# Kernel optimization log

Hardware: AMD Instinct MI355X
Metric: run time of the kernel (lower is better)

Reference implementation:

```python
import jax, jax.numpy as jnp
import numpy as np

N_NODES = 50000
N_EDGES = 600000
HIDDEN = 128
OUT = 64


def gcn_conv(x, edge_index, W, b, num_nodes):
    """PyG GCNConv: out = D^-1/2 (A+I) D^-1/2 (x W) + b, deg computed on A+I."""
    src, dst = edge_index[0], edge_index[1]
    loops = jnp.arange(num_nodes, dtype=src.dtype)
    src_f = jnp.concatenate([src, loops])  # [E+N]
    dst_f = jnp.concatenate([dst, loops])
    deg = jax.ops.segment_sum(jnp.ones_like(dst_f, dtype=x.dtype), dst_f,
                              num_segments=num_nodes)  # in-degree incl. self-loop
    dinv = jnp.where(deg > 0, jax.lax.rsqrt(deg), 0.0)
    norm = dinv[src_f] * dinv[dst_f]  # [E+N]
    xw = x @ W  # [N, out]
    msg = xw[src_f] * norm[:, None]  # gather + scale
    out = jax.ops.segment_sum(msg, dst_f, num_segments=num_nodes)
    return out + b


def setup_inputs() -> dict:
    key = jax.random.key(0)
    k1, k2, k3, k4, k5 = jax.random.split(key, 5)
    x = jax.random.normal(k1, (N_NODES, HIDDEN), dtype=jnp.float32)
    edge_index = jax.random.randint(k2, (2, N_EDGES), 0, N_NODES, dtype=jnp.int64)
    # Glorot-style init, scale just for numerics
    W1 = jax.random.normal(k3, (HIDDEN, HIDDEN), dtype=jnp.float32) / np.sqrt(HIDDEN)
    b1 = jnp.zeros((HIDDEN,), dtype=jnp.float32)
    W2 = jax.random.normal(k4, (HIDDEN, OUT), dtype=jnp.float32) / np.sqrt(HIDDEN)
    b2 = jnp.zeros((OUT,), dtype=jnp.float32)
    return {"x": x, "edge_index": edge_index, "W1": W1, "b1": b1, "W2": W2, "b2": b2}


def reference(x, edge_index, W1, b1, W2, b2):
    # dropout is identity in eval mode
    h = jax.nn.relu(gcn_conv(x, edge_index, W1, b1, N_NODES))
    out = gcn_conv(h, edge_index, W2, b2, N_NODES)
    return out
```

## Files before the change

### kernel.cpp

```cpp
#include <hip/hip_runtime.h>
#include <hip/hip_bf16.h>


#define NN 50000
#define NE 600000
#define HID 128
#define OUTD 64
#define NP 50048
#define CAP 64
#define MT 3125
#define BINSH 7
#define BINN 128
#define NBIN 391
#define BCAP 2048
#define EPB1 4096
#define G1 147
#define GEMM1B 1564

typedef __attribute__((ext_vector_type(8))) short short8v;
typedef __attribute__((ext_vector_type(4))) float f32x4;

__device__ __forceinline__ float b2f(ushort u) {
  return __uint_as_float(((uint)u) << 16);
}
__device__ __forceinline__ float bf_lo(uint v) { return __uint_as_float(v << 16); }
__device__ __forceinline__ float bf_hi(uint v) { return __uint_as_float(v & 0xffff0000u); }
__device__ __forceinline__ ushort f2b(float x) {
  __hip_bfloat16 h = __float2bfloat16(x);
  return *reinterpret_cast<ushort*>(&h);
}

__global__ __launch_bounds__(256) void k_init(const float* __restrict__ W1,
                                              const float* __restrict__ W2,
                                              ushort* __restrict__ W1t,
                                              ushort* __restrict__ W2t,
                                              int* __restrict__ bincnt) {
  int b = blockIdx.x;
  int t = threadIdx.x;
  if (b < 64) {
    int idx = b * 256 + t;
    int n = idx >> 7, k = idx & 127;
    W1t[idx] = f2b(W1[k * HID + n]);
  } else if (b < 96) {
    int idx = (b - 64) * 256 + t;
    int n = idx >> 7, k = idx & 127;
    W2t[idx] = f2b(W2[k * OUTD + n]);
  } else {
    for (int i = t; i < NBIN; i += 256) bincnt[i] = 0;
  }
}

__global__ __launch_bounds__(256) void k_bin1(const int* __restrict__ src,
                                              const int* __restrict__ dst,
                                              int* __restrict__ bincnt,
                                              int2* __restrict__ binbuf) {
  __shared__ int hist[NBIN];
  __shared__ int base[NBIN];
  __shared__ int lcur[NBIN];
  const int t = threadIdx.x;
  const int e0 = blockIdx.x * EPB1;
  for (int i = t; i < NBIN; i += 256) { hist[i] = 0; lcur[i] = 0; }
  __syncthreads();

  int2 er[16];
#pragma unroll
  for (int k = 0; k < 16; ++k) {
    int idx = k * 256 + t;
    int e = e0 + idx;
    int2 p = make_int2(0, -1);
    if (e < NE) p = make_int2(src[e], dst[e]);
    er[k] = p;
    if (p.y >= 0) atomicAdd(&hist[p.y >> BINSH], 1);
  }
  __syncthreads();
  for (int i = t; i < NBIN; i += 256) {
    int h = hist[i];
    base[i] = h ? atomicAdd(&bincnt[i], h) : 0;
  }
  __syncthreads();
#pragma unroll
  for (int k = 0; k < 16; ++k) {
    int2 p = er[k];
    if (p.y >= 0) {
      int b = p.y >> BINSH;
      int loc = atomicAdd(&lcur[b], 1);
      int gpos = base[b] + loc;
      if (gpos < BCAP) binbuf[(size_t)b * BCAP + gpos] = p;
    }
  }
}

__global__ __launch_bounds__(256) void k_bin2_gemm1(const int* __restrict__ bincnt,
                                                    const int2* __restrict__ binbuf,
                                                    int* __restrict__ cnt,
                                                    float* __restrict__ dinv,
                                                    int* __restrict__ bucket,
                                                    const float* __restrict__ x,
                                                    const ushort* __restrict__ W1t,
                                                    ushort* __restrict__ C) {
  int blk = blockIdx.x;
  if (blk < NBIN) {
    __shared__ int lcnt[BINN];
    __shared__ int lbuck[BINN][CAP];
    const int t = threadIdx.x;
    for (int i = t; i < BINN; i += 256) lcnt[i] = 0;
    __syncthreads();
    const int nodes0 = blk << BINSH;
    const int bc = min(bincnt[blk], BCAP);
    const int2* bb = binbuf + (size_t)blk * BCAP;
    for (int i = t; i < bc; i += 256) {
      int2 p = bb[i];
      int c = p.y & (BINN - 1);
      int slot = atomicAdd(&lcnt[c], 1);
      if (slot < CAP) lbuck[c][slot] = p.x;
    }
    __syncthreads();
    for (int i = t; i < BINN * CAP; i += 256) {
      int c = i >> 6;
      int sl = i & (CAP - 1);
      bucket[(size_t)(nodes0 + c) * CAP + sl] = lbuck[c][sl];
    }
    for (int i = t; i < BINN; i += 256) {
      int node = nodes0 + i;
      if (node < NN) {
        int m = min(lcnt[i], CAP);
        cnt[node] = m;
        dinv[node] = rsqrtf((float)m + 1.0f);
      }
    }
    return;
  }

  int gb = blk - NBIN;
  const int wave = threadIdx.x >> 6;
  const int lane = threadIdx.x & 63;
  const int mt = (gb >> 1) * 4 + wave;
  if (mt >= MT) return;
  const int colh = gb & 1;
  const int r16 = lane & 15;
  const int kg = lane >> 4;
  const int row = mt * 16 + r16;

  short8v afr[4];
  const float* ap = x + (size_t)row * HID;
#pragma unroll
  for (int s = 0; s < 4; ++s) {
    float4 lo = *(const float4*)(ap + s * 32 + kg * 8);
    float4 hi = *(const float4*)(ap + s * 32 + kg * 8 + 4);
    short8v v;
    v[0] = (short)f2b(lo.x); v[1] = (short)f2b(lo.y);
    v[2] = (short)f2b(lo.z); v[3] = (short)f2b(lo.w);
    v[4] = (short)f2b(hi.x); v[5] = (short)f2b(hi.y);
    v[6] = (short)f2b(hi.z); v[7] = (short)f2b(hi.w);
    afr[s] = v;
  }

  f32x4 acc[4];
#pragma unroll
  for (int nt = 0; nt < 4; ++nt) acc[nt] = (f32x4){0.f, 0.f, 0.f, 0.f};

#pragma unroll
  for (int nt = 0; nt < 4; ++nt) {
    const ushort* bp = W1t + (size_t)(colh * 64 + nt * 16 + r16) * HID;
#pragma unroll
    for (int s = 0; s < 4; ++s) {
      short8v bfr = *reinterpret_cast<const short8v*>(bp + s * 32 + kg * 8);
      acc[nt] = __builtin_amdgcn_mfma_f32_16x16x32_bf16(afr[s], bfr, acc[nt], 0, 0, 0);
    }
  }

#pragma unroll
  for (int nt = 0; nt < 4; ++nt) {
#pragma unroll
    for (int r = 0; r < 4; ++r) {
      int orow = mt * 16 + kg * 4 + r;
      C[(size_t)orow * HID + colh * 64 + nt * 16 + r16] = f2b(acc[nt][r]);
    }
  }
}

__global__ __launch_bounds__(256) void k_gather_w_f(const int* __restrict__ cnt,
                                                    const float* __restrict__ dinv,
                                                    const int* __restrict__ bucket,
                                                    const ushort* __restrict__ feat,
                                                    const float* __restrict__ bias,
                                                    const ushort* __restrict__ W2t,
                                                    ushort* __restrict__ hw2u) {
  __shared__ uint hl[16][68];
  const int wave = threadIdx.x >> 6;
  const int lane = threadIdx.x & 63;
  const int nbase = blockIdx.x * 16;
  const uint* fu = (const uint*)feat;
  const float bia0 = bias[2 * lane];
  const float bia1 = bias[2 * lane + 1];

  int elq[4], dgq[4];
  float dnq[4];
#pragma unroll
  for (int q = 0; q < 4; ++q) {
    int node = nbase + wave * 4 + q;
    elq[q] = bucket[(size_t)node * CAP + lane];
    dgq[q] = cnt[node];
    dnq[q] = dinv[node];
  }

#pragma unroll
  for (int q = 0; q < 4; ++q) {
    const int node = nbase + wave * 4 + q;
    const int el = elq[q];
    const int deg = dgq[q];
    const float dd = dnq[q];
    uint sv = fu[((size_t)node << 6) + lane];
    float a0 = dd * dd * bf_lo(sv), b0 = dd * dd * bf_hi(sv);
    float a1 = 0.f, b1 = 0.f, a2 = 0.f, b2 = 0.f, a3 = 0.f, b3 = 0.f;
    int j = 0;
    for (; j + 8 <= deg; j += 8) {
      int s0 = __shfl(el, j + 0), s1 = __shfl(el, j + 1);
      int s2 = __shfl(el, j + 2), s3 = __shfl(el, j + 3);
      int s4 = __shfl(el, j + 4), s5 = __shfl(el, j + 5);
      int s6 = __shfl(el, j + 6), s7 = __shfl(el, j + 7);
      float w0 = dd * dinv[s0], w1 = dd * dinv[s1];
      float w2 = dd * dinv[s2], w3 = dd * dinv[s3];
      float w4 = dd * dinv[s4], w5 = dd * dinv[s5];
      float w6 = dd * dinv[s6], w7 = dd * dinv[s7];
      uint v0 = fu[((size_t)s0 << 6) + lane], v1 = fu[((size_t)s1 << 6) + lane];
      uint v2 = fu[((size_t)s2 << 6) + lane], v3 = fu[((size_t)s3 << 6) + lane];
      uint v4 = fu[((size_t)s4 << 6) + lane], v5 = fu[((size_t)s5 << 6) + lane];
      uint v6 = fu[((size_t)s6 << 6) + lane], v7 = fu[((size_t)s7 << 6) + lane];
      a0 += w0 * bf_lo(v0); b0 += w0 * bf_hi(v0);
      a1 += w1 * bf_lo(v1); b1 += w1 * bf_hi(v1);
      a2 += w2 * bf_lo(v2); b2 += w2 * bf_hi(v2);
      a3 += w3 * bf_lo(v3); b3 += w3 * bf_hi(v3);
      a0 += w4 * bf_lo(v4); b0 += w4 * bf_hi(v4);
      a1 += w5 * bf_lo(v5); b1 += w5 * bf_hi(v5);
      a2 += w6 * bf_lo(v6); b2 += w6 * bf_hi(v6);
      a3 += w7 * bf_lo(v7); b3 += w7 * bf_hi(v7);
    }
    for (; j + 4 <= deg; j += 4) {
      int s0 = __shfl(el, j + 0), s1 = __shfl(el, j + 1);
      int s2 = __shfl(el, j + 2), s3 = __shfl(el, j + 3);
      float w0 = dd * dinv[s0], w1 = dd * dinv[s1];
      float w2 = dd * dinv[s2], w3 = dd * dinv[s3];
      uint v0 = fu[((size_t)s0 << 6) + lane], v1 = fu[((size_t)s1 << 6) + lane];
      uint v2 = fu[((size_t)s2 << 6) + lane], v3 = fu[((size_t)s3 << 6) + lane];
      a0 += w0 * bf_lo(v0); b0 += w0 * bf_hi(v0);
      a1 += w1 * bf_lo(v1); b1 += w1 * bf_hi(v1);
      a2 += w2 * bf_lo(v2); b2 += w2 * bf_hi(v2);
      a3 += w3 * bf_lo(v3); b3 += w3 * bf_hi(v3);
    }
    for (; j < deg; ++j) {
      int s = __shfl(el, j);
      float w = dd * dinv[s];
      uint v = fu[((size_t)s << 6) + lane];
      a0 += w * bf_lo(v); b0 += w * bf_hi(v);
    }
    float r0 = fmaxf((a0 + a1) + (a2 + a3) + bia0, 0.f);
    float r1 = fmaxf((b0 + b1) + (b2 + b3) + bia1, 0.f);
    hl[wave * 4 + q][lane] = (uint)f2b(r0) | ((uint)f2b(r1) << 16);
  }
  __syncthreads();

  const int r16 = lane & 15;
  const int kg = lane >> 4;
  const ushort* hrow = (const ushort*)&hl[r16][0];
  short8v afr[4];
#pragma unroll
  for (int s = 0; s < 4; ++s)
    afr[s] = *reinterpret_cast<const short8v*>(hrow + s * 32 + kg * 8);
  f32x4 acc = (f32x4){0.f, 0.f, 0.f, 0.f};
  const ushort* bp = W2t + (size_t)(wave * 16 + r16) * HID;
#pragma unroll
  for (int s = 0; s < 4; ++s) {
    short8v bfr = *reinterpret_cast<const short8v*>(bp + s * 32 + kg * 8);
    acc = __builtin_amdgcn_mfma_f32_16x16x32_bf16(afr[s], bfr, acc, 0, 0, 0);
  }
#pragma unroll
  for (int r = 0; r < 4; ++r)
    hw2u[(size_t)(nbase + kg * 4 + r) * OUTD + wave * 16 + r16] = f2b(acc[r]);
}

__global__ __launch_bounds__(256) void k_gather_n(const int* __restrict__ cnt,
                                                  const float* __restrict__ dinv,
                                                  const int* __restrict__ bucket,
                                                  const ushort* __restrict__ feat,
                                                  const float* __restrict__ bias,
                                                  float* __restrict__ out) {
  int node = blockIdx.x * 4 + (threadIdx.x >> 6);
  int lane = threadIdx.x & 63;
  const int el = bucket[(size_t)node * CAP + lane];
  const int deg = cnt[node];
  const float dd = dinv[node];
  float a0 = dd * dd * b2f(feat[((size_t)node << 6) + lane]);
  float a1 = 0.f, a2 = 0.f, a3 = 0.f;
  int j = 0;
  for (; j + 8 <= deg; j += 8) {
    int s0 = __shfl(el, j + 0), s1 = __shfl(el, j + 1);
    int s2 = __shfl(el, j + 2), s3 = __shfl(el, j + 3);
    int s4 = __shfl(el, j + 4), s5 = __shfl(el, j + 5);
    int s6 = __shfl(el, j + 6), s7 = __shfl(el, j + 7);
    float w0 = dd * dinv[s0], w1 = dd * dinv[s1];
    float w2 = dd * dinv[s2], w3 = dd * dinv[s3];
    float w4 = dd * dinv[s4], w5 = dd * dinv[s5];
    float w6 = dd * dinv[s6], w7 = dd * dinv[s7];
    float v0 = b2f(feat[((size_t)s0 << 6) + lane]);
    float v1 = b2f(feat[((size_t)s1 << 6) + lane]);
    float v2 = b2f(feat[((size_t)s2 << 6) + lane]);
    float v3 = b2f(feat[((size_t)s3 << 6) + lane]);
    float v4 = b2f(feat[((size_t)s4 << 6) + lane]);
    float v5 = b2f(feat[((size_t)s5 << 6) + lane]);
    float v6 = b2f(feat[((size_t)s6 << 6) + lane]);
    float v7 = b2f(feat[((size_t)s7 << 6) + lane]);
    a0 += w0 * v0; a1 += w1 * v1; a2 += w2 * v2; a3 += w3 * v3;
    a0 += w4 * v4; a1 += w5 * v5; a2 += w6 * v6; a3 += w7 * v7;
  }
  for (; j + 4 <= deg; j += 4) {
    int s0 = __shfl(el, j + 0), s1 = __shfl(el, j + 1);
    int s2 = __shfl(el, j + 2), s3 = __shfl(el, j + 3);
    float w0 = dd * dinv[s0], w1 = dd * dinv[s1];
    float w2 = dd * dinv[s2], w3 = dd * dinv[s3];
    float v0 = b2f(feat[((size_t)s0 << 6) + lane]);
    float v1 = b2f(feat[((size_t)s1 << 6) + lane]);
    float v2 = b2f(feat[((size_t)s2 << 6) + lane]);
    float v3 = b2f(feat[((size_t)s3 << 6) + lane]);
    a0 += w0 * v0; a1 += w1 * v1; a2 += w2 * v2; a3 += w3 * v3;
  }
  for (; j < deg; ++j) {
    int s = __shfl(el, j);
    a0 += (dd * dinv[s]) * b2f(feat[((size_t)s << 6) + lane]);
  }
  out[(size_t)node * OUTD + lane] = (a0 + a1) + (a2 + a3) + bias[lane];
}


extern "C" void kernel_launch(void* const* d_in, const int* in_sizes, int n_in,
                              void* d_out, int out_size, void* d_ws, size_t ws_size,
                              hipStream_t stream) {
  const float* x  = (const float*)d_in[0];
  const int*   ei = (const int*)d_in[1];
  const float* W1 = (const float*)d_in[2];
  const float* b1 = (const float*)d_in[3];
  const float* W2 = (const float*)d_in[4];
  const float* b2 = (const float*)d_in[5];
  float* out = (float*)d_out;

  const int* src = ei;
  const int* dst = ei + NE;

  int*    cnt    = (int*)d_ws;
  float*  dinv   = (float*)(cnt + NP);
  int*    bucket = (int*)(dinv + NP);
  ushort* xw1u   = (ushort*)(bucket + (size_t)NP * CAP);
  ushort* hw2u   = xw1u + (size_t)NN * HID;
  ushort* W1t    = hw2u + (size_t)NN * OUTD;
  ushort* W2t    = W1t + 16384;
  int*    bincnt = (int*)(W2t + 8192);
  int2*   binbuf = (int2*)(bincnt + NBIN + 1);

  k_init<<<97, 256, 0, stream>>>(W1, W2, W1t, W2t, bincnt);
  k_bin1<<<G1, 256, 0, stream>>>(src, dst, bincnt, binbuf);
  k_bin2_gemm1<<<NBIN + GEMM1B, 256, 0, stream>>>(bincnt, binbuf, cnt, dinv,
                                                  bucket, x, W1t, xw1u);
  k_gather_w_f<<<MT, 256, 0, stream>>>(cnt, dinv, bucket, xw1u, b1, W2t, hw2u);
  k_gather_n<<<NN / 4, 256, 0, stream>>>(cnt, dinv, bucket, hw2u, b2, out);
}
```

Baseline: 109.6 us.

## Split fused layer-1 gather and GEMM2 into separate gather and GEMM kernels

```diff
diff --git a/kernel.cpp b/kernel.cpp
--- a/kernel.cpp
+++ b/kernel.cpp
@@ -179,104 +179,107 @@
   }
 }
 
-__global__ __launch_bounds__(256) void k_gather_w_f(const int* __restrict__ cnt,
-                                                    const float* __restrict__ dinv,
-                                                    const int* __restrict__ bucket,
-                                                    const ushort* __restrict__ feat,
-                                                    const float* __restrict__ bias,
-                                                    const ushort* __restrict__ W2t,
-                                                    ushort* __restrict__ hw2u) {
-  __shared__ uint hl[16][68];
+__global__ __launch_bounds__(256) void k_gather_w(const int* __restrict__ cnt,
+                                                  const float* __restrict__ dinv,
+                                                  const int* __restrict__ bucket,
+                                                  const ushort* __restrict__ feat,
+                                                  const float* __restrict__ bias,
+                                                  ushort* __restrict__ hu) {
   const int wave = threadIdx.x >> 6;
   const int lane = threadIdx.x & 63;
-  const int nbase = blockIdx.x * 16;
+  const int node = blockIdx.x * 4 + wave;
   const uint* fu = (const uint*)feat;
-  const float bia0 = bias[2 * lane];
-  const float bia1 = bias[2 * lane + 1];
-
-  int elq[4], dgq[4];
-  float dnq[4];
-#pragma unroll
-  for (int q = 0; q < 4; ++q) {
-    int node = nbase + wave * 4 + q;
-    elq[q] = bucket[(size_t)node * CAP + lane];
-    dgq[q] = cnt[node];
-    dnq[q] = dinv[node];
-  }
-
-#pragma unroll
-  for (int q = 0; q < 4; ++q) {
-    const int node = nbase + wave * 4 + q;
-    const int el = elq[q];
-    const int deg = dgq[q];
-    const float dd = dnq[q];
-    uint sv = fu[((size_t)node << 6) + lane];
-    float a0 = dd * dd * bf_lo(sv), b0 = dd * dd * bf_hi(sv);
-    float a1 = 0.f, b1 = 0.f, a2 = 0.f, b2 = 0.f, a3 = 0.f, b3 = 0.f;
-    int j = 0;
-    for (; j + 8 <= deg; j += 8) {
-      int s0 = __shfl(el, j + 0), s1 = __shfl(el, j + 1);
-      int s2 = __shfl(el, j + 2), s3 = __shfl(el, j + 3);
-      int s4 = __shfl(el, j + 4), s5 = __shfl(el, j + 5);
-      int s6 = __shfl(el, j + 6), s7 = __shfl(el, j + 7);
-      float w0 = dd * dinv[s0], w1 = dd * dinv[s1];
-      float w2 = dd * dinv[s2], w3 = dd * dinv[s3];
-      float w4 = dd * dinv[s4], w5 = dd * dinv[s5];
-      float w6 = dd * dinv[s6], w7 = dd * dinv[s7];
-      uint v0 = fu[((size_t)s0 << 6) + lane], v1 = fu[((size_t)s1 << 6) + lane];
-      uint v2 = fu[((size_t)s2 << 6) + lane], v3 = fu[((size_t)s3 << 6) + lane];
-      uint v4 = fu[((size_t)s4 << 6) + lane], v5 = fu[((size_t)s5 << 6) + lane];
-      uint v6 = fu[((size_t)s6 << 6) + lane], v7 = fu[((size_t)s7 << 6) + lane];
-      a0 += w0 * bf_lo(v0); b0 += w0 * bf_hi(v0);
-      a1 += w1 * bf_lo(v1); b1 += w1 * bf_hi(v1);
-      a2 += w2 * bf_lo(v2); b2 += w2 * bf_hi(v2);
-      a3 += w3 * bf_lo(v3); b3 += w3 * bf_hi(v3);
-      a0 += w4 * bf_lo(v4); b0 += w4 * bf_hi(v4);
-      a1 += w5 * bf_lo(v5); b1 += w5 * bf_hi(v5);
-      a2 += w6 * bf_lo(v6); b2 += w6 * bf_hi(v6);
-      a3 += w7 * bf_lo(v7); b3 += w7 * bf_hi(v7);
-    }
-    for (; j + 4 <= deg; j += 4) {
-      int s0 = __shfl(el, j + 0), s1 = __shfl(el, j + 1);
-      int s2 = __shfl(el, j + 2), s3 = __shfl(el, j + 3);
-      float w0 = dd * dinv[s0], w1 = dd * dinv[s1];
-      float w2 = dd * dinv[s2], w3 = dd * dinv[s3];
-      uint v0 = fu[((size_t)s0 << 6) + lane], v1 = fu[((size_t)s1 << 6) + lane];
-      uint v2 = fu[((size_t)s2 << 6) + lane], v3 = fu[((size_t)s3 << 6) + lane];
-      a0 += w0 * bf_lo(v0); b0 += w0 * bf_hi(v0);
-      a1 += w1 * bf_lo(v1); b1 += w1 * bf_hi(v1);
-      a2 += w2 * bf_lo(v2); b2 += w2 * bf_hi(v2);
-      a3 += w3 * bf_lo(v3); b3 += w3 * bf_hi(v3);
-    }
-    for (; j < deg; ++j) {
-      int s = __shfl(el, j);
-      float w = dd * dinv[s];
-      uint v = fu[((size_t)s << 6) + lane];
-      a0 += w * bf_lo(v); b0 += w * bf_hi(v);
-    }
-    float r0 = fmaxf((a0 + a1) + (a2 + a3) + bia0, 0.f);
-    float r1 = fmaxf((b0 + b1) + (b2 + b3) + bia1, 0.f);
-    hl[wave * 4 + q][lane] = (uint)f2b(r0) | ((uint)f2b(r1) << 16);
-  }
-  __syncthreads();
-
+
+  const int el = bucket[(size_t)node * CAP + lane];
+  const int deg = cnt[node];
+  const float dd = dinv[node];
+  uint sv = fu[((size_t)node << 6) + lane];
+  float a0 = dd * dd * bf_lo(sv), b0 = dd * dd * bf_hi(sv);
+  float a1 = 0.f, b1 = 0.f, a2 = 0.f, b2 = 0.f, a3 = 0.f, b3 = 0.f;
+  int j = 0;
+  for (; j + 8 <= deg; j += 8) {
+    int s0 = __shfl(el, j + 0), s1 = __shfl(el, j + 1);
+    int s2 = __shfl(el, j + 2), s3 = __shfl(el, j + 3);
+    int s4 = __shfl(el, j + 4), s5 = __shfl(el, j + 5);
+    int s6 = __shfl(el, j + 6), s7 = __shfl(el, j + 7);
+    float w0 = dd * dinv[s0], w1 = dd * dinv[s1];
+    float w2 = dd * dinv[s2], w3 = dd * dinv[s3];
+    float w4 = dd * dinv[s4], w5 = dd * dinv[s5];
+    float w6 = dd * dinv[s6], w7 = dd * dinv[s7];
+    uint v0 = fu[((size_t)s0 << 6) + lane], v1 = fu[((size_t)s1 << 6) + lane];
+    uint v2 = fu[((size_t)s2 << 6) + lane], v3 = fu[((size_t)s3 << 6) + lane];
+    uint v4 = fu[((size_t)s4 << 6) + lane], v5 = fu[((size_t)s5 << 6) + lane];
+    uint v6 = fu[((size_t)s6 << 6) + lane], v7 = fu[((size_t)s7 << 6) + lane];
+    a0 += w0 * bf_lo(v0); b0 += w0 * bf_hi(v0);
+    a1 += w1 * bf_lo(v1); b1 += w1 * bf_hi(v1);
+    a2 += w2 * bf_lo(v2); b2 += w2 * bf_hi(v2);
+    a3 += w3 * bf_lo(v3); b3 += w3 * bf_hi(v3);
+    a0 += w4 * bf_lo(v4); b0 += w4 * bf_hi(v4);
+    a1 += w5 * bf_lo(v5); b1 += w5 * bf_hi(v5);
+    a2 += w6 * bf_lo(v6); b2 += w6 * bf_hi(v6);
+    a3 += w7 * bf_lo(v7); b3 += w7 * bf_hi(v7);
+  }
+  for (; j + 4 <= deg; j += 4) {
+    int s0 = __shfl(el, j + 0), s1 = __shfl(el, j + 1);
+    int s2 = __shfl(el, j + 2), s3 = __shfl(el, j + 3);
+    float w0 = dd * dinv[s0], w1 = dd * dinv[s1];
+    float w2 = dd * dinv[s2], w3 = dd * dinv[s3];
+    uint v0 = fu[((size_t)s0 << 6) + lane], v1 = fu[((size_t)s1 << 6) + lane];
+    uint v2 = fu[((size_t)s2 << 6) + lane], v3 = fu[((size_t)s3 << 6) + lane];
+    a0 += w0 * bf_lo(v0); b0 += w0 * bf_hi(v0);
+    a1 += w1 * bf_lo(v1); b1 += w1 * bf_hi(v1);
+    a2 += w2 * bf_lo(v2); b2 += w2 * bf_hi(v2);
+    a3 += w3 * bf_lo(v3); b3 += w3 * bf_hi(v3);
+  }
+  for (; j < deg; ++j) {
+    int s = __shfl(el, j);
+    float w = dd * dinv[s];
+    uint v = fu[((size_t)s << 6) + lane];
+    a0 += w * bf_lo(v); b0 += w * bf_hi(v);
+  }
+  float r0 = fmaxf((a0 + a1) + (a2 + a3) + bias[2 * lane], 0.f);
+  float r1 = fmaxf((b0 + b1) + (b2 + b3) + bias[2 * lane + 1], 0.f);
+  ((uint*)hu)[((size_t)node << 6) + lane] = (uint)f2b(r0) | ((uint)f2b(r1) << 16);
+}
+
+__global__ __launch_bounds__(256) void k_gemm2(const ushort* __restrict__ hu,
+                                               const ushort* __restrict__ W2t,
+                                               ushort* __restrict__ C) {
+  const int wave = threadIdx.x >> 6;
+  const int lane = threadIdx.x & 63;
+  const int mt = blockIdx.x * 4 + wave;
   const int r16 = lane & 15;
   const int kg = lane >> 4;
-  const ushort* hrow = (const ushort*)&hl[r16][0];
+  const int row = mt * 16 + r16;
+
   short8v afr[4];
+  const ushort* ap = hu + (size_t)row * HID;
 #pragma unroll
   for (int s = 0; s < 4; ++s)
-    afr[s] = *reinterpret_cast<const short8v*>(hrow + s * 32 + kg * 8);
-  f32x4 acc = (f32x4){0.f, 0.f, 0.f, 0.f};
-  const ushort* bp = W2t + (size_t)(wave * 16 + r16) * HID;
-#pragma unroll
-  for (int s = 0; s < 4; ++s) {
-    short8v bfr = *reinterpret_cast<const short8v*>(bp + s * 32 + kg * 8);
-    acc = __builtin_amdgcn_mfma_f32_16x16x32_bf16(afr[s], bfr, acc, 0, 0, 0);
-  }
-#pragma unroll
-  for (int r = 0; r < 4; ++r)
-    hw2u[(size_t)(nbase + kg * 4 + r) * OUTD + wave * 16 + r16] = f2b(acc[r]);
+    afr[s] = *reinterpret_cast<const short8v*>(ap + s * 32 + kg * 8);
+
+  f32x4 acc[4];
+#pragma unroll
+  for (int nt = 0; nt < 4; ++nt) acc[nt] = (f32x4){0.f, 0.f, 0.f, 0.f};
+
+#pragma unroll
+  for (int nt = 0; nt < 4; ++nt) {
+    const ushort* bp = W2t + (size_t)(nt * 16 + r16) * HID;
+#pragma unroll
+    for (int s = 0; s < 4; ++s) {
+      short8v bfr = *reinterpret_cast<const short8v*>(bp + s * 32 + kg * 8);
+      acc[nt] = __builtin_amdgcn_mfma_f32_16x16x32_bf16(afr[s], bfr, acc[nt], 0, 0, 0);
+    }
+  }
+
+#pragma unroll
+  for (int nt = 0; nt < 4; ++nt) {
+#pragma unroll
+    for (int r = 0; r < 4; ++r) {
+      int orow = mt * 16 + kg * 4 + r;
+      C[(size_t)orow * OUTD + nt * 16 + r16] = f2b(acc[nt][r]);
+    }
+  }
 }
 
 __global__ __launch_bounds__(256) void k_gather_n(const int* __restrict__ cnt,
@@ -350,7 +353,8 @@
   float*  dinv   = (float*)(cnt + NP);
   int*    bucket = (int*)(dinv + NP);
   ushort* xw1u   = (ushort*)(bucket + (size_t)NP * CAP);
-  ushort* hw2u   = xw1u + (size_t)NN * HID;
+  ushort* hu     = xw1u + (size_t)NN * HID;
+  ushort* hw2u   = hu + (size_t)NN * HID;
   ushort* W1t    = hw2u + (size_t)NN * OUTD;
   ushort* W2t    = W1t + 16384;
   int*    bincnt = (int*)(W2t + 8192);
@@ -360,6 +364,7 @@
   k_bin1<<<G1, 256, 0, stream>>>(src, dst, bincnt, binbuf);
   k_bin2_gemm1<<<NBIN + GEMM1B, 256, 0, stream>>>(bincnt, binbuf, cnt, dinv,
                                                   bucket, x, W1t, xw1u);
-  k_gather_w_f<<<MT, 256, 0, stream>>>(cnt, dinv, bucket, xw1u, b1, W2t, hw2u);
+  k_gather_w<<<NN / 4, 256, 0, stream>>>(cnt, dinv, bucket, xw1u, b1, hu);
+  k_gemm2<<<MT / 4 + 1, 256, 0, stream>>>(hu, W2t, hw2u);
   k_gather_n<<<NN / 4, 256, 0, stream>>>(cnt, dinv, bucket, hw2u, b2, out);
 }
```

Result: no change. 108.1 us, median of 2 (-1.4%).
